# Optimization experiments

Measured on AMD Instinct MI355X. Metric: run time of the kernel, lower is better.

The kernel has to match this reference:

```python
import jax, jax.numpy as jnp
import numpy as np

B, S, H = 16, 4096, 1024

def setup_inputs() -> dict:
    key = jax.random.key(0)
    k = jax.random.split(key, 6)
    return {
        "query": jax.random.normal(k[0], (B, 1, H), dtype=jnp.float32),
        "proj_key": jax.random.normal(k[1], (B, S, H), dtype=jnp.float32),
        "value": jax.random.normal(k[2], (B, S, 2 * H), dtype=jnp.float32),
        "Wq": jax.random.normal(k[3], (H, H), dtype=jnp.float32) * (1.0 / np.sqrt(H)),
        "we": jax.random.normal(k[4], (H,), dtype=jnp.float32) * (1.0 / np.sqrt(H)),
        "mask": jax.random.randint(k[5], (B, S), 0, 2, dtype=jnp.int32),
    }

def reference(query, proj_key, value, Wq, we, mask):
    # query: [B,1,H]; torch Linear(no bias): y = x @ W^T
    q = jnp.einsum('bqh,oh->bqo', query, Wq)            # [B,1,H]
    e = jnp.tanh(q + proj_key)                          # [B,S,H] (broadcast over S)
    scores = jnp.einsum('bsh,h->bs', e, we)             # energy_layer -> [B,S]
    scores = jnp.where(mask == 0, -jnp.inf, scores)
    alphas = jax.nn.softmax(scores, axis=-1)            # [B,S]
    context = jnp.einsum('bs,bsd->bd', alphas, value)   # bmm([B,1,S],[B,S,2H])
    return context[:, None, :], alphas[:, None, :]
```

## Files before the change

### kernel.cpp

```cpp
#include <hip/hip_runtime.h>
#include <math.h>

#define BATCH 16
#define SEQ   4096
#define HDIM  1024
#define DV    2048
#define NCH2  64
#define SCH2  (SEQ / NCH2)

typedef float vf4 __attribute__((ext_vector_type(4)));

__device__ __forceinline__ float tanh_fast(float x) {
    float e = __expf(2.0f * x);
    return 1.0f - 2.0f * __builtin_amdgcn_rcpf(1.0f + e);
}

__device__ __forceinline__ float4 ntload4(const float4* p) {
    vf4 v = __builtin_nontemporal_load((const vf4*)p);
    return make_float4(v.x, v.y, v.z, v.w);
}

__global__ __launch_bounds__(256) void k1_q(const float* __restrict__ query,
                                            const float* __restrict__ Wq,
                                            float* __restrict__ qout) {
    int wave = threadIdx.x >> 6;
    int lane = threadIdx.x & 63;
    int o = blockIdx.x * 4 + wave;
    const float4* wq4 = (const float4*)(Wq + (size_t)o * HDIM);
    float4 w[4];
#pragma unroll
    for (int k = 0; k < 4; ++k) w[k] = wq4[k * 64 + lane];
#pragma unroll
    for (int b = 0; b < BATCH; ++b) {
        const float4* q4 = (const float4*)(query + b * HDIM);
        float acc = 0.f;
#pragma unroll
        for (int k = 0; k < 4; ++k) {
            float4 q = q4[k * 64 + lane];
            acc += w[k].x * q.x + w[k].y * q.y + w[k].z * q.z + w[k].w * q.w;
        }
#pragma unroll
        for (int off = 32; off; off >>= 1) acc += __shfl_down(acc, off, 64);
        if (lane == 0) qout[b * HDIM + o] = acc;
    }
}

__global__ __launch_bounds__(256) void kf_fused(const float* __restrict__ pk,
                                                const float* __restrict__ qv,
                                                const float* __restrict__ we,
                                                const int* __restrict__ mask,
                                                const float* __restrict__ value,
                                                float* __restrict__ scores,
                                                float* __restrict__ partial) {
    int bid = blockIdx.x;
    int b = bid >> 6;
    int c = bid & (NCH2 - 1);
    int s0 = c * SCH2;
    int t = threadIdx.x;
    int wave = t >> 6;
    int lane = t & 63;

    __shared__ float s_sc[SCH2];
    __shared__ float s_a[SCH2];
    __shared__ int   s_list[SCH2];
    __shared__ int   s_nact;

    if (t < SCH2) {
        int r = b * SEQ + s0 + t;
        int pred = (mask[r] != 0);
        unsigned long long bal = __ballot(pred);
        if (pred) {
            int pos = __popcll(bal & ((1ull << lane) - 1ull));
            s_list[pos] = t;
        } else {
            s_sc[t] = -INFINITY;
            scores[r] = -INFINITY;
        }
        if (lane == 0) s_nact = __popcll(bal);
    }

    const float4* q4  = (const float4*)(qv + b * HDIM);
    const float4* we4 = (const float4*)we;
    float4 qr[4], wr[4];
#pragma unroll
    for (int k = 0; k < 4; ++k) {
        qr[k] = q4[k * 64 + lane];
        wr[k] = we4[k * 64 + lane];
    }
    __syncthreads();
    int nact = s_nact;

    for (int j = wave; j < nact; j += 4) {
        int s = s_list[j];
        int r = b * SEQ + s0 + s;
        const float4* row = (const float4*)(pk + (size_t)r * HDIM);
        float acc = 0.f;
#pragma unroll
        for (int k = 0; k < 4; ++k) {
            float4 p = ntload4(row + k * 64 + lane);
            acc += tanh_fast(p.x + qr[k].x) * wr[k].x;
            acc += tanh_fast(p.y + qr[k].y) * wr[k].y;
            acc += tanh_fast(p.z + qr[k].z) * wr[k].z;
            acc += tanh_fast(p.w + qr[k].w) * wr[k].w;
        }
#pragma unroll
        for (int off = 32; off; off >>= 1) acc += __shfl_down(acc, off, 64);
        if (lane == 0) {
            s_sc[s] = acc;
            scores[r] = acc;
        }
    }
    __syncthreads();

    float mc = -INFINITY;
#pragma unroll 8
    for (int s = 0; s < SCH2; ++s) mc = fmaxf(mc, s_sc[s]);
    if (t < SCH2)
        s_a[t] = (s_sc[t] == -INFINITY || mc == -INFINITY) ? 0.f : __expf(s_sc[t] - mc);
    __syncthreads();

    const float4* v4 = (const float4*)(value + (size_t)b * SEQ * DV);
    float4 a0 = make_float4(0.f, 0.f, 0.f, 0.f);
    float4 a1 = make_float4(0.f, 0.f, 0.f, 0.f);
    for (int j = 0; j < nact; ++j) {
        int s = s_list[j];
        float a = s_a[s];
        const float4* vr = v4 + (size_t)(s0 + s) * (DV / 4);
        float4 u = ntload4(vr + t);
        float4 v = ntload4(vr + t + 256);
        a0.x += a * u.x; a0.y += a * u.y; a0.z += a * u.z; a0.w += a * u.w;
        a1.x += a * v.x; a1.y += a * v.y; a1.z += a * v.z; a1.w += a * v.w;
    }
    float4* pout = (float4*)(partial + (size_t)bid * DV);
    pout[t] = a0;
    pout[t + 256] = a1;
}

__global__ __launch_bounds__(256) void kz_final(const float* __restrict__ scores,
                                                const float* __restrict__ partial,
                                                float* __restrict__ ctx,
                                                float* __restrict__ alphas) {
    int bid = blockIdx.x;
    int b = bid >> 4;
    int q = bid & 15;
    int t = threadIdx.x;
    int wave = t >> 6;
    int lane = t & 63;

    __shared__ float s_raw[SEQ];
    __shared__ float s_g[NCH2];
    __shared__ float red[8];
    __shared__ float s_half[128];

    const float4* sc4 = (const float4*)(scores + (size_t)b * SEQ);
    float4* raw4 = (float4*)s_raw;
#pragma unroll
    for (int i = 0; i < 4; ++i) raw4[t + i * 256] = sc4[t + i * 256];
    __syncthreads();

    float m = -INFINITY;
#pragma unroll
    for (int i = 0; i < 16; ++i) m = fmaxf(m, s_raw[t + i * 256]);
#pragma unroll
    for (int off = 32; off; off >>= 1) m = fmaxf(m, __shfl_down(m, off, 64));
    if (lane == 0) red[wave] = m;
    __syncthreads();
    m = fmaxf(fmaxf(red[0], red[1]), fmaxf(red[2], red[3]));

    float z = 0.f;
#pragma unroll
    for (int i = 0; i < 16; ++i) {
        float v = s_raw[t + i * 256];
        z += (v == -INFINITY) ? 0.f : __expf(v - m);
    }
#pragma unroll
    for (int off = 32; off; off >>= 1) z += __shfl_down(z, off, 64);
    if (lane == 0) red[4 + wave] = z;
    __syncthreads();
    float Z = red[4] + red[5] + red[6] + red[7];
    float inv = 1.0f / Z;

    if (t < NCH2) {
        float mcv = -INFINITY;
#pragma unroll 8
        for (int j = 0; j < SCH2; ++j)
            mcv = fmaxf(mcv, s_raw[t * SCH2 + ((j + t) & (SCH2 - 1))]);
        s_g[t] = (mcv == -INFINITY) ? 0.f : __expf(mcv - m);
    }

    {
        float v = s_raw[q * 256 + t];
        float e = (v == -INFINITY) ? 0.f : __expf(v - m);
        alphas[(size_t)b * SEQ + q * 256 + t] = e * inv;
    }
    __syncthreads();

    int col = q * 128 + (t & 127);
    int half = t >> 7;
    float sum = 0.f;
    const float* pbase = partial + (size_t)b * NCH2 * DV + col;
#pragma unroll 4
    for (int cc = half * 32; cc < half * 32 + 32; ++cc) {
        float g = s_g[cc];
        if (g != 0.f) sum += g * pbase[(size_t)cc * DV];
    }
    if (half == 1) s_half[t & 127] = sum;
    __syncthreads();
    if (half == 0)
        ctx[(size_t)b * DV + col] = (sum + s_half[t]) * inv;
}

__global__ __launch_bounds__(256) void k2_scores(const float* __restrict__ pk,
                                                 const float* __restrict__ qv,
                                                 const float* __restrict__ we,
                                                 const int* __restrict__ mask,
                                                 float* __restrict__ scores) {
    int wave = threadIdx.x >> 6;
    int lane = threadIdx.x & 63;
    int r = blockIdx.x * 4 + wave;
    int b = r >> 12;
    if (mask[r] == 0) { if (lane == 0) scores[r] = -INFINITY; return; }
    const float4* row = (const float4*)(pk + (size_t)r * HDIM);
    const float4* q4  = (const float4*)(qv + b * HDIM);
    const float4* we4 = (const float4*)we;
    float acc = 0.f;
#pragma unroll
    for (int k = 0; k < 4; ++k) {
        int idx = k * 64 + lane;
        float4 p = row[idx];
        float4 q = q4[idx];
        float4 w = we4[idx];
        acc += tanh_fast(p.x + q.x) * w.x;
        acc += tanh_fast(p.y + q.y) * w.y;
        acc += tanh_fast(p.z + q.z) * w.z;
        acc += tanh_fast(p.w + q.w) * w.w;
    }
#pragma unroll
    for (int off = 32; off; off >>= 1) acc += __shfl_down(acc, off, 64);
    if (lane == 0) scores[r] = acc;
}

__global__ __launch_bounds__(256) void k3_softmax(const float* __restrict__ scores,
                                                  float* __restrict__ alphas) {
    int b = blockIdx.x;
    int t = threadIdx.x;
    const float* sc = scores + b * SEQ;
    float loc[16];
    float m = -INFINITY;
#pragma unroll
    for (int i = 0; i < 16; ++i) { loc[i] = sc[t + i * 256]; m = fmaxf(m, loc[i]); }
#pragma unroll
    for (int off = 32; off; off >>= 1) m = fmaxf(m, __shfl_down(m, off, 64));
    __shared__ float redm[4];
    if ((t & 63) == 0) redm[t >> 6] = m;
    __syncthreads();
    m = fmaxf(fmaxf(redm[0], redm[1]), fmaxf(redm[2], redm[3]));
    float sum = 0.f;
#pragma unroll
    for (int i = 0; i < 16; ++i) {
        loc[i] = (loc[i] == -INFINITY) ? 0.f : __expf(loc[i] - m);
        sum += loc[i];
    }
#pragma unroll
    for (int off = 32; off; off >>= 1) sum += __shfl_down(sum, off, 64);
    __shared__ float reds[4];
    if ((t & 63) == 0) reds[t >> 6] = sum;
    __syncthreads();
    float inv = 1.0f / (reds[0] + reds[1] + reds[2] + reds[3]);
#pragma unroll
    for (int i = 0; i < 16; ++i) alphas[b * SEQ + t + i * 256] = loc[i] * inv;
}

__global__ __launch_bounds__(256) void k4_atomic(const float* __restrict__ value,
                                                 const float* __restrict__ alphas,
                                                 float* __restrict__ ctx) {
    int bid = blockIdx.x;
    int ch = bid & 31;
    int dt = (bid >> 5) & 1;
    int b  = bid >> 6;
    int t  = threadIdx.x;
    const float4* v4 = (const float4*)(value + (size_t)b * SEQ * DV + dt * 1024);
    const float* al = alphas + b * SEQ + ch * 128;
    float4 acc = make_float4(0.f, 0.f, 0.f, 0.f);
    for (int s = 0; s < 128; ++s) {
        float a = al[s];
        if (a != 0.f) {
            float4 v = v4[(size_t)(ch * 128 + s) * (DV / 4) + t];
            acc.x += a * v.x; acc.y += a * v.y; acc.z += a * v.z; acc.w += a * v.w;
        }
    }
    float* dst = ctx + (size_t)b * DV + dt * 1024 + t * 4;
    atomicAdd(dst + 0, acc.x);
    atomicAdd(dst + 1, acc.y);
    atomicAdd(dst + 2, acc.z);
    atomicAdd(dst + 3, acc.w);
}

extern "C" void kernel_launch(void* const* d_in, const int* in_sizes, int n_in,
                              void* d_out, int out_size, void* d_ws, size_t ws_size,
                              hipStream_t stream) {
    const float* query = (const float*)d_in[0];
    const float* pk    = (const float*)d_in[1];
    const float* value = (const float*)d_in[2];
    const float* Wq    = (const float*)d_in[3];
    const float* we    = (const float*)d_in[4];
    const int*   mask  = (const int*)d_in[5];

    float* out    = (float*)d_out;
    float* ctx    = out;
    float* alphas = out + BATCH * DV;

    float* ws     = (float*)d_ws;
    float* qws    = ws;
    float* scores = ws + BATCH * HDIM;
    float* partial = scores + BATCH * SEQ;

    k1_q<<<HDIM / 4, 256, 0, stream>>>(query, Wq, qws);

    size_t need = (size_t)(BATCH * HDIM + BATCH * SEQ + BATCH * NCH2 * DV) * sizeof(float);
    if (ws_size >= need) {
        kf_fused<<<BATCH * NCH2, 256, 0, stream>>>(pk, qws, we, mask, value, scores, partial);
        kz_final<<<BATCH * 16, 256, 0, stream>>>(scores, partial, ctx, alphas);
    } else {
        k2_scores<<<(BATCH * SEQ) / 4, 256, 0, stream>>>(pk, qws, we, mask, scores);
        k3_softmax<<<BATCH, 256, 0, stream>>>(scores, alphas);
        (void)hipMemsetAsync(ctx, 0, (size_t)BATCH * DV * sizeof(float), stream);
        k4_atomic<<<BATCH * 64, 256, 0, stream>>>(value, alphas, ctx);
    }
}
```

Measured before the change: 95.28 us.

## Emit per-chunk max and sum in fused kernel; halve chunk count

The fused score and value kernel now reduces each chunk's max and exp-sum with wave shuffles and writes them to workspace. The final kernel then combines these 32 per-chunk statistics instead of loading and re-reducing all 4096 scores per block. The chunk count per batch drops from 64 to 32, giving fewer partial context rows to write and re-read but only 512 blocks with more serial value rows each. The final kernel also recomputes the chunk scaling exponentials inline rather than caching them in shared memory.

```diff
diff --git a/kernel.cpp b/kernel.cpp
--- a/kernel.cpp
+++ b/kernel.cpp
@@ -5,8 +5,8 @@
 #define SEQ   4096
 #define HDIM  1024
 #define DV    2048
-#define NCH2  64
-#define SCH2  (SEQ / NCH2)
+#define NCH   32
+#define SCH   (SEQ / NCH)
 
 typedef float vf4 __attribute__((ext_vector_type(4)));
 
@@ -51,32 +51,44 @@
                                                 const int* __restrict__ mask,
                                                 const float* __restrict__ value,
                                                 float* __restrict__ scores,
-                                                float* __restrict__ partial) {
+                                                float* __restrict__ partial,
+                                                float* __restrict__ chunkm,
+                                                float* __restrict__ chunkz) {
     int bid = blockIdx.x;
-    int b = bid >> 6;
-    int c = bid & (NCH2 - 1);
-    int s0 = c * SCH2;
+    int b = bid >> 5;
+    int c = bid & (NCH - 1);
+    int s0 = c * SCH;
     int t = threadIdx.x;
     int wave = t >> 6;
     int lane = t & 63;
 
-    __shared__ float s_sc[SCH2];
-    __shared__ float s_a[SCH2];
-    __shared__ int   s_list[SCH2];
+    __shared__ float s_sc[SCH];
+    __shared__ float s_a[SCH];
+    __shared__ int   s_list[SCH];
     __shared__ int   s_nact;
-
-    if (t < SCH2) {
-        int r = b * SEQ + s0 + t;
-        int pred = (mask[r] != 0);
-        unsigned long long bal = __ballot(pred);
-        if (pred) {
-            int pos = __popcll(bal & ((1ull << lane) - 1ull));
-            s_list[pos] = t;
+    __shared__ float red[8];
+
+    if (t < 64) {
+        int r0 = b * SEQ + s0 + t;
+        int p0 = (mask[r0] != 0);
+        unsigned long long b0 = __ballot(p0);
+        int n0 = __popcll(b0);
+        if (p0) {
+            s_list[__popcll(b0 & ((1ull << lane) - 1ull))] = t;
         } else {
             s_sc[t] = -INFINITY;
-            scores[r] = -INFINITY;
-        }
-        if (lane == 0) s_nact = __popcll(bal);
+            scores[r0] = -INFINITY;
+        }
+        int r1 = b * SEQ + s0 + 64 + t;
+        int p1 = (mask[r1] != 0);
+        unsigned long long b1 = __ballot(p1);
+        if (p1) {
+            s_list[n0 + __popcll(b1 & ((1ull << lane) - 1ull))] = 64 + t;
+        } else {
+            s_sc[64 + t] = -INFINITY;
+            scores[r1] = -INFINITY;
+        }
+        if (lane == 0) s_nact = n0 + __popcll(b1);
     }
 
     const float4* q4  = (const float4*)(qv + b * HDIM);
@@ -112,12 +124,28 @@
     }
     __syncthreads();
 
-    float mc = -INFINITY;
-#pragma unroll 8
-    for (int s = 0; s < SCH2; ++s) mc = fmaxf(mc, s_sc[s]);
-    if (t < SCH2)
-        s_a[t] = (s_sc[t] == -INFINITY || mc == -INFINITY) ? 0.f : __expf(s_sc[t] - mc);
-    __syncthreads();
+    float mval = (t < SCH) ? s_sc[t] : -INFINITY;
+    float mr = mval;
+#pragma unroll
+    for (int off = 32; off; off >>= 1) mr = fmaxf(mr, __shfl_down(mr, off, 64));
+    if (lane == 0) red[wave] = mr;
+    __syncthreads();
+    float mc = fmaxf(fmaxf(red[0], red[1]), fmaxf(red[2], red[3]));
+
+    float av = 0.f;
+    if (t < SCH) {
+        av = (mval == -INFINITY || mc == -INFINITY) ? 0.f : __expf(mval - mc);
+        s_a[t] = av;
+    }
+    float zr = av;
+#pragma unroll
+    for (int off = 32; off; off >>= 1) zr += __shfl_down(zr, off, 64);
+    if (lane == 0) red[4 + wave] = zr;
+    __syncthreads();
+    if (t == 0) {
+        chunkm[bid] = mc;
+        chunkz[bid] = red[4] + red[5];
+    }
 
     const float4* v4 = (const float4*)(value + (size_t)b * SEQ * DV);
     float4 a0 = make_float4(0.f, 0.f, 0.f, 0.f);
@@ -138,71 +166,53 @@
 
 __global__ __launch_bounds__(256) void kz_final(const float* __restrict__ scores,
                                                 const float* __restrict__ partial,
+                                                const float* __restrict__ chunkm,
+                                                const float* __restrict__ chunkz,
                                                 float* __restrict__ ctx,
                                                 float* __restrict__ alphas) {
     int bid = blockIdx.x;
     int b = bid >> 4;
     int q = bid & 15;
     int t = threadIdx.x;
-    int wave = t >> 6;
-    int lane = t & 63;
-
-    __shared__ float s_raw[SEQ];
-    __shared__ float s_g[NCH2];
-    __shared__ float red[8];
+
+    __shared__ float s_m[NCH];
+    __shared__ float s_z[NCH];
     __shared__ float s_half[128];
 
-    const float4* sc4 = (const float4*)(scores + (size_t)b * SEQ);
-    float4* raw4 = (float4*)s_raw;
-#pragma unroll
-    for (int i = 0; i < 4; ++i) raw4[t + i * 256] = sc4[t + i * 256];
+    if (t < NCH) {
+        s_m[t] = chunkm[b * NCH + t];
+        s_z[t] = chunkz[b * NCH + t];
+    }
     __syncthreads();
 
     float m = -INFINITY;
 #pragma unroll
-    for (int i = 0; i < 16; ++i) m = fmaxf(m, s_raw[t + i * 256]);
-#pragma unroll
-    for (int off = 32; off; off >>= 1) m = fmaxf(m, __shfl_down(m, off, 64));
-    if (lane == 0) red[wave] = m;
-    __syncthreads();
-    m = fmaxf(fmaxf(red[0], red[1]), fmaxf(red[2], red[3]));
-
-    float z = 0.f;
-#pragma unroll
-    for (int i = 0; i < 16; ++i) {
-        float v = s_raw[t + i * 256];
-        z += (v == -INFINITY) ? 0.f : __expf(v - m);
-    }
-#pragma unroll
-    for (int off = 32; off; off >>= 1) z += __shfl_down(z, off, 64);
-    if (lane == 0) red[4 + wave] = z;
-    __syncthreads();
-    float Z = red[4] + red[5] + red[6] + red[7];
+    for (int i = 0; i < NCH; ++i) m = fmaxf(m, s_m[i]);
+    float Z = 0.f;
+#pragma unroll
+    for (int i = 0; i < NCH; ++i) {
+        float mi = s_m[i];
+        if (mi != -INFINITY) Z += s_z[i] * __expf(mi - m);
+    }
     float inv = 1.0f / Z;
 
-    if (t < NCH2) {
-        float mcv = -INFINITY;
-#pragma unroll 8
-        for (int j = 0; j < SCH2; ++j)
-            mcv = fmaxf(mcv, s_raw[t * SCH2 + ((j + t) & (SCH2 - 1))]);
-        s_g[t] = (mcv == -INFINITY) ? 0.f : __expf(mcv - m);
-    }
-
     {
-        float v = s_raw[q * 256 + t];
-        float e = (v == -INFINITY) ? 0.f : __expf(v - m);
+        float sc = scores[(size_t)b * SEQ + q * 256 + t];
+        float e = (sc == -INFINITY) ? 0.f : __expf(sc - m);
         alphas[(size_t)b * SEQ + q * 256 + t] = e * inv;
     }
-    __syncthreads();
 
     int col = q * 128 + (t & 127);
     int half = t >> 7;
     float sum = 0.f;
-    const float* pbase = partial + (size_t)b * NCH2 * DV + col;
+    const float* pbase = partial + (size_t)b * NCH * DV + col;
 #pragma unroll 4
-    for (int cc = half * 32; cc < half * 32 + 32; ++cc) {
-        float g = s_g[cc];
-        if (g != 0.f) sum += g * pbase[(size_t)cc * DV];
+    for (int cc = half * 16; cc < half * 16 + 16; ++cc) {
+        float mi = s_m[cc];
+        if (mi != -INFINITY) {
+            float g = __expf(mi - m);
+            sum += g * pbase[(size_t)cc * DV];
+        }
     }
     if (half == 1) s_half[t & 127] = sum;
     __syncthreads();
@@ -310,17 +320,22 @@
     float* ctx    = out;
     float* alphas = out + BATCH * DV;
 
-    float* ws     = (float*)d_ws;
-    float* qws    = ws;
-    float* scores = ws + BATCH * HDIM;
-    float* partial = scores + BATCH * SEQ;
+    float* ws      = (float*)d_ws;
+    float* qws     = ws;
+    float* scores  = ws + BATCH * HDIM;
+    float* chunkm  = scores + BATCH * SEQ;
+    float* chunkz  = chunkm + BATCH * NCH;
+    float* partial = chunkz + BATCH * NCH;
 
     k1_q<<<HDIM / 4, 256, 0, stream>>>(query, Wq, qws);
 
-    size_t need = (size_t)(BATCH * HDIM + BATCH * SEQ + BATCH * NCH2 * DV) * sizeof(float);
+    size_t need = (size_t)(BATCH * HDIM + BATCH * SEQ + 2 * BATCH * NCH
+                           + (size_t)BATCH * NCH * DV) * sizeof(float);
     if (ws_size >= need) {
-        kf_fused<<<BATCH * NCH2, 256, 0, stream>>>(pk, qws, we, mask, value, scores, partial);
-        kz_final<<<BATCH * 16, 256, 0, stream>>>(scores, partial, ctx, alphas);
+        kf_fused<<<BATCH * NCH, 256, 0, stream>>>(pk, qws, we, mask, value,
+                                                  scores, partial, chunkm, chunkz);
+        kz_final<<<BATCH * 16, 256, 0, stream>>>(scores, partial, chunkm, chunkz,
+                                                 ctx, alphas);
     } else {
         k2_scores<<<(BATCH * SEQ) / 4, 256, 0, stream>>>(pk, qws, we, mask, scores);
         k3_softmax<<<BATCH, 256, 0, stream>>>(scores, alphas);
```

Measured after the change: 109.9 us. 15.3% more time.
